# Kernel optimization log

Measured on AMD Instinct MI355X. Metric: run time of the kernel, lower is better.

Reference implementation:

```python
import jax, jax.numpy as jnp
import numpy as np

B, S, D, H = 4, 2048, 1024, 16
HD = D // H  # 64


def setup_inputs() -> dict:
    key = jax.random.key(0)
    ks = jax.random.split(key, 8)
    std = 0.02
    return {
        "input_tensor": jax.random.normal(ks[0], (B, S, D), jnp.float32),
        "attention_mask": jnp.zeros((B, 1, 1, S), jnp.float32),
        "Wq": jax.random.normal(ks[1], (D, D), jnp.float32) * std,
        "bq": jnp.zeros((D,), jnp.float32),
        "Wk": jax.random.normal(ks[2], (D, D), jnp.float32) * std,
        "bk": jnp.zeros((D,), jnp.float32),
        "Wv": jax.random.normal(ks[3], (D, D), jnp.float32) * std,
        "bv": jnp.zeros((D,), jnp.float32),
    }


def reference(input_tensor, attention_mask, Wq, bq, Wk, bk, Wv, bv):
    # QKV projections: [B,S,D]
    q = input_tensor @ Wq + bq
    k = input_tensor @ Wk + bk
    v = input_tensor @ Wv + bv
    # split heads -> [B,H,S,hd]
    split = lambda x: x.reshape(B, S, H, HD).transpose(0, 2, 1, 3)
    q, k, v = split(q), split(k), split(v)
    scale = HD ** (-0.5)
    # [B,H,S,S]
    scores = jnp.einsum("bhqd,bhkd->bhqk", q * scale, k) + attention_mask
    probs = jax.nn.softmax(scores, axis=-1)  # dropout skipped (train=False)
    out = jnp.einsum("bhqk,bhkd->bhqd", probs, v)
    return out.transpose(0, 2, 1, 3).reshape(B, S, D)
```

## Files before the change

### kernel.cpp

```cpp
#include <hip/hip_runtime.h>
#include <hip/hip_bf16.h>

#define BB 4
#define SS 2048
#define DD 1024
#define HH 16
#define HDD 64
#define MM (BB*SS)
#define KVB 64
#define NT (SS/KVB)

typedef __attribute__((ext_vector_type(4))) float f32x4;
typedef __attribute__((ext_vector_type(2))) _Float16 f16x2;
typedef __attribute__((ext_vector_type(4))) _Float16 f16x4;
typedef __attribute__((ext_vector_type(8))) _Float16 f16x8;
typedef __attribute__((ext_vector_type(2))) __fp16 fp16x2_builtin;
typedef __attribute__((ext_vector_type(4))) unsigned int u32x4;

#define LOG2E 1.4426950408889634f
#define QSCALE (0.125f * LOG2E)

__device__ inline float fast_exp2(float x) {
  return __builtin_exp2f(x);
}

__device__ inline f16x2 pk2(float a, float b) {
  union { fp16x2_builtin b2; f16x2 h2; } u;
  u.b2 = __builtin_amdgcn_cvt_pkrtz(a, b);
  return u.h2;
}

__device__ inline f32x4 mfma16(f16x8 a, f16x8 b, f32x4 c) {
  return __builtin_amdgcn_mfma_f32_16x16x32_f16(a, b, c, 0, 0, 0);
}

__device__ inline f16x8 comb(f16x4 lo, f16x4 hi) {
  return __builtin_shufflevector(lo, hi, 0, 1, 2, 3, 4, 5, 6, 7);
}

__device__ inline f16x8 ld_frag(const _Float16* p) {
  f16x4 lo = *reinterpret_cast<const f16x4*>(p);
  f16x4 hi = *reinterpret_cast<const f16x4*>(p + 16);
  return comb(lo, hi);
}

__global__ __launch_bounds__(256) void cvt_x_kernel(
    const float* __restrict__ x, _Float16* __restrict__ xh, int n4) {
  int i = blockIdx.x * 256 + threadIdx.x;
  int stride = gridDim.x * 256;
  for (; i < n4; i += stride) {
    f32x4 v = reinterpret_cast<const f32x4*>(x)[i];
    reinterpret_cast<f16x4*>(xh)[i] = __builtin_convertvector(v, f16x4);
  }
}

__global__ __launch_bounds__(256) void mask_scale_kernel(
    const float* __restrict__ m, float* __restrict__ o, int n) {
  int i = blockIdx.x * 256 + threadIdx.x;
  if (i < n) o[i] = m[i] * LOG2E;
}

__global__ __launch_bounds__(256) void cvt_w_kernel(
    const float* __restrict__ Wq, const float* __restrict__ Wk,
    const float* __restrict__ Wv, _Float16* __restrict__ Wt) {
  __shared__ float tile[32][33];
  const int w = blockIdx.z;
  const float* W = (w == 0) ? Wq : (w == 1) ? Wk : Wv;
  _Float16* outp = Wt + (size_t)w * DD * DD;
  const int n0 = blockIdx.x * 32, k0 = blockIdx.y * 32;
  const int tx = threadIdx.x, ty = threadIdx.y;
#pragma unroll
  for (int i = 0; i < 32; i += 8)
    tile[ty + i][tx] = W[(size_t)(k0 + ty + i) * DD + n0 + tx];
  __syncthreads();
#pragma unroll
  for (int i = 0; i < 32; i += 8)
    outp[(size_t)(n0 + ty + i) * DD + k0 + tx] = (_Float16)tile[tx][ty + i];
}

#define LDT 40
__global__ __launch_bounds__(256) void qkv_gemm_kernel(
    const _Float16* __restrict__ Xh, const _Float16* __restrict__ Wt,
    const float* __restrict__ bq, const float* __restrict__ bk, const float* __restrict__ bv,
    _Float16* __restrict__ Qh, _Float16* __restrict__ Kh,
    _Float16* __restrict__ Vt) {
  __shared__ _Float16 At[128 * LDT];
  __shared__ _Float16 Bt[128 * LDT];
  const int w = blockIdx.y;
  const _Float16* Wp = Wt + (size_t)w * DD * DD;
  const int tid = threadIdx.x;
  const int lane = tid & 63, wave = tid >> 6;
  const int g = lane >> 4, r = lane & 15;
  const int mt = blockIdx.x & 63, nt = blockIdx.x >> 6;
  const int m0 = mt * 128, n0 = nt * 128;
  const int wr = wave >> 1, wc = wave & 1;

  f32x4 acc[4][4];
#pragma unroll
  for (int i = 0; i < 4; ++i)
#pragma unroll
    for (int j = 0; j < 4; ++j) { f32x4 z = {0.f, 0.f, 0.f, 0.f}; acc[i][j] = z; }

  const int r0 = tid >> 2, c0 = (tid & 3) * 8;
  const int r1 = (tid + 256) >> 2, c1 = (tid & 3) * 8;

  u32x4 a0 = *reinterpret_cast<const u32x4*>(&Xh[(size_t)(m0 + r0) * DD + c0]);
  u32x4 a1 = *reinterpret_cast<const u32x4*>(&Xh[(size_t)(m0 + r1) * DD + c1]);
  u32x4 b0 = *reinterpret_cast<const u32x4*>(&Wp[(size_t)(n0 + r0) * DD + c0]);
  u32x4 b1 = *reinterpret_cast<const u32x4*>(&Wp[(size_t)(n0 + r1) * DD + c1]);

  for (int kt = 0; kt < DD; kt += 32) {
    __syncthreads();
    *reinterpret_cast<u32x4*>(&At[r0 * LDT + c0]) = a0;
    *reinterpret_cast<u32x4*>(&At[r1 * LDT + c1]) = a1;
    *reinterpret_cast<u32x4*>(&Bt[r0 * LDT + c0]) = b0;
    *reinterpret_cast<u32x4*>(&Bt[r1 * LDT + c1]) = b1;
    __syncthreads();

    const bool more = (kt + 32) < DD;
    if (more) {
      a0 = *reinterpret_cast<const u32x4*>(&Xh[(size_t)(m0 + r0) * DD + kt + 32 + c0]);
      a1 = *reinterpret_cast<const u32x4*>(&Xh[(size_t)(m0 + r1) * DD + kt + 32 + c1]);
      b0 = *reinterpret_cast<const u32x4*>(&Wp[(size_t)(n0 + r0) * DD + kt + 32 + c0]);
      b1 = *reinterpret_cast<const u32x4*>(&Wp[(size_t)(n0 + r1) * DD + kt + 32 + c1]);
    }

    f16x8 af[4], bf[4];
#pragma unroll
    for (int ms = 0; ms < 4; ++ms)
      af[ms] = ld_frag(&At[(wr * 64 + ms * 16 + r) * LDT + 4 * g]);
#pragma unroll
    for (int ns = 0; ns < 4; ++ns)
      bf[ns] = ld_frag(&Bt[(wc * 64 + ns * 16 + r) * LDT + 4 * g]);
#pragma unroll
    for (int ms = 0; ms < 4; ++ms)
#pragma unroll
      for (int ns = 0; ns < 4; ++ns)
        acc[ms][ns] = mfma16(af[ms], bf[ns], acc[ms][ns]);
  }

  const float* bias = (w == 0) ? bq : (w == 1) ? bk : bv;
#pragma unroll
  for (int ns = 0; ns < 4; ++ns) {
    const int gcol = n0 + wc * 64 + ns * 16 + r;
    const float bv_ = bias[gcol];
    const int h = gcol >> 6, d = gcol & 63;
#pragma unroll
    for (int ms = 0; ms < 4; ++ms) {
#pragma unroll
      for (int reg = 0; reg < 4; ++reg) {
        const int grow = m0 + wr * 64 + ms * 16 + 4 * g + reg;
        const float v = acc[ms][ns][reg] + bv_;
        const int bb = grow >> 11, s = grow & 2047;
        const int bh = bb * HH + h;
        if (w == 0)
          Qh[((size_t)bh * SS + s) * HDD + d] = (_Float16)(v * QSCALE);
        else if (w == 1)
          Kh[((size_t)bh * SS + s) * HDD + d] = (_Float16)v;
        else {
          const int w5 = s & 31;
          const int pos = (w5 & 16) ? ((((w5 >> 2) & 3) << 3) + 4 + (w5 & 3))
                                    : (((w5 >> 2) << 3) + (w5 & 3));
          const int sp = (s & ~31) | pos;
          Vt[((size_t)bh * HDD + d) * SS + sp] = (_Float16)v;
        }
      }
    }
  }
}

__global__ __launch_bounds__(256) void attn_kernel(
    const _Float16* __restrict__ Qh, const _Float16* __restrict__ Kh,
    const _Float16* __restrict__ Vg, const float* __restrict__ maskSc,
    float* __restrict__ out) {
  __shared__ _Float16 Ks[2][KVB * 64];
  __shared__ _Float16 Vs[2][KVB * 64];
  const int bh = blockIdx.y;
  const int b = bh >> 4, h = bh & 15;
  const int tid = threadIdx.x, lane = tid & 63, wave = tid >> 6;
  const int g = lane >> 4, r = lane & 15;
  const int q0 = blockIdx.x * 128 + wave * 32;

  f16x8 qf[2][2];
#pragma unroll
  for (int qs = 0; qs < 2; ++qs) {
    const _Float16* Qp = Qh + ((size_t)bh * SS + q0 + qs * 16 + r) * HDD;
    qf[qs][0] = *reinterpret_cast<const f16x8*>(Qp + 8 * g);
    qf[qs][1] = *reinterpret_cast<const f16x8*>(Qp + 32 + 8 * g);
  }

  float m_run[2] = {-1e30f, -1e30f};
  float l_run[2] = {0.f, 0.f};
  f32x4 acc[2][4];
#pragma unroll
  for (int qs = 0; qs < 2; ++qs)
#pragma unroll
    for (int i = 0; i < 4; ++i) { f32x4 z = {0.f, 0.f, 0.f, 0.f}; acc[qs][i] = z; }

  const _Float16* Kg = Kh + (size_t)bh * SS * HDD;
  const _Float16* Vgb = Vg + (size_t)bh * HDD * SS;
  const float* mbase = maskSc + b * SS;

  const int srow = lane >> 3;
  const int scol = (lane & 7) * 8;
  u32x4 kreg[2], vreg[2];

  auto stage_load = [&](int kk) {
#pragma unroll
    for (int i = 0; i < 2; ++i) {
      const int row = wave * 16 + i * 8 + srow;
      kreg[i] = *reinterpret_cast<const u32x4*>(Kg + (size_t)(kk + row) * HDD + scol);
      vreg[i] = *reinterpret_cast<const u32x4*>(Vgb + (size_t)row * SS + kk + scol);
    }
  };
  auto stage_write = [&](int buf) {
#pragma unroll
    for (int i = 0; i < 2; ++i) {
      const int row = wave * 16 + i * 8 + srow;
      const int sw = (row & 7) << 3;
      *reinterpret_cast<u32x4*>(&Ks[buf][row * 64 + (scol ^ sw)]) = kreg[i];
      *reinterpret_cast<u32x4*>(&Vs[buf][row * 64 + (scol ^ sw)]) = vreg[i];
    }
  };

  int cur = 0;
  stage_load(0);
  stage_write(0);
  __syncthreads();

  for (int t = 0; t < NT; ++t) {
    const int kk = t * KVB;
    const bool more = (t + 1) < NT;
    if (more) stage_load(kk + KVB);

    f32x4 mk[2][2];
#pragma unroll
    for (int sg = 0; sg < 2; ++sg)
#pragma unroll
      for (int h16 = 0; h16 < 2; ++h16)
        mk[sg][h16] = *reinterpret_cast<const f32x4*>(mbase + kk + sg * 32 + h16 * 16 + 4 * g);

#pragma unroll
    for (int sg = 0; sg < 2; ++sg) {
      f32x4 st[2][2];
#pragma unroll
      for (int h16 = 0; h16 < 2; ++h16) {
        const int row = sg * 32 + h16 * 16 + r;
        const int sw = (row & 7) << 3;
        const _Float16* kb = &Ks[cur][row * 64];
        f16x8 a0 = *reinterpret_cast<const f16x8*>(kb + ((8 * g) ^ sw));
        f16x8 a1 = *reinterpret_cast<const f16x8*>(kb + ((32 + 8 * g) ^ sw));
        f32x4 z = {0.f, 0.f, 0.f, 0.f};
        st[0][h16] = mfma16(a1, qf[0][1], mfma16(a0, qf[0][0], z));
        st[1][h16] = mfma16(a1, qf[1][1], mfma16(a0, qf[1][0], z));
      }

      f16x8 pf[2];
#pragma unroll
      for (int qs = 0; qs < 2; ++qs) {
        float p0[4], p1[4];
        float pmax = -1e30f;
#pragma unroll
        for (int j = 0; j < 4; ++j) {
          const float s0 = st[qs][0][j] + mk[sg][0][j];
          const float s1 = st[qs][1][j] + mk[sg][1][j];
          p0[j] = s0; p1[j] = s1;
          pmax = fmaxf(pmax, fmaxf(s0, s1));
        }
        if (!__all(pmax <= m_run[qs] + 8.0f)) {
          float tm = fmaxf(pmax, __shfl_xor(pmax, 16));
          tm = fmaxf(tm, __shfl_xor(tm, 32));
          const float m_new = fmaxf(m_run[qs], tm);
          const float corr = fast_exp2(m_run[qs] - m_new);
          l_run[qs] *= corr;
#pragma unroll
          for (int i = 0; i < 4; ++i) acc[qs][i] = acc[qs][i] * corr;
          m_run[qs] = m_new;
        }
        const float mr = m_run[qs];
        float rs = 0.f;
#pragma unroll
        for (int j = 0; j < 4; ++j) {
          p0[j] = fast_exp2(p0[j] - mr);
          p1[j] = fast_exp2(p1[j] - mr);
          rs += p0[j] + p1[j];
        }
        l_run[qs] += rs;
        union { f16x2 h2[4]; f16x8 v; } u;
        u.h2[0] = pk2(p0[0], p0[1]);
        u.h2[1] = pk2(p0[2], p0[3]);
        u.h2[2] = pk2(p1[0], p1[1]);
        u.h2[3] = pk2(p1[2], p1[3]);
        pf[qs] = u.v;
      }

#pragma unroll
      for (int dsb = 0; dsb < 4; ++dsb) {
        const int row = dsb * 16 + r;
        const int sw = (row & 7) << 3;
        f16x8 vf = *reinterpret_cast<const f16x8*>(
            &Vs[cur][row * 64 + ((sg * 32 + 8 * g) ^ sw)]);
        acc[0][dsb] = mfma16(vf, pf[0], acc[0][dsb]);
        acc[1][dsb] = mfma16(vf, pf[1], acc[1][dsb]);
      }
    }

    if (more) stage_write(cur ^ 1);
    __syncthreads();
    cur ^= 1;
  }

#pragma unroll
  for (int qs = 0; qs < 2; ++qs) {
    float l = l_run[qs];
    l += __shfl_xor(l, 16);
    l += __shfl_xor(l, 32);
    const float inv = 1.0f / l;
    float* op = out + ((size_t)b * SS + q0 + qs * 16 + r) * DD + h * HDD;
#pragma unroll
    for (int dsb = 0; dsb < 4; ++dsb) {
      f32x4 o = { acc[qs][dsb][0] * inv, acc[qs][dsb][1] * inv,
                  acc[qs][dsb][2] * inv, acc[qs][dsb][3] * inv };
      *reinterpret_cast<f32x4*>(op + dsb * 16 + 4 * g) = o;
    }
  }
}

extern "C" void kernel_launch(void* const* d_in, const int* in_sizes, int n_in,
                              void* d_out, int out_size, void* d_ws, size_t ws_size,
                              hipStream_t stream) {
  const float* x    = (const float*)d_in[0];
  const float* mask = (const float*)d_in[1];
  const float* Wq   = (const float*)d_in[2];
  const float* bq   = (const float*)d_in[3];
  const float* Wk   = (const float*)d_in[4];
  const float* bk   = (const float*)d_in[5];
  const float* Wv   = (const float*)d_in[6];
  const float* bv   = (const float*)d_in[7];
  float* out = (float*)d_out;

  _Float16* Xh = (_Float16*)d_ws;
  _Float16* Wt = Xh + (size_t)MM * DD;
  _Float16* Qh = Wt + (size_t)3 * DD * DD;
  _Float16* Kh = Qh + (size_t)MM * DD;
  _Float16* Vt = Kh + (size_t)MM * DD;
  float* maskSc = (float*)(Vt + (size_t)MM * DD);

  cvt_x_kernel<<<dim3(2048), dim3(256), 0, stream>>>(x, Xh, MM * DD / 4);
  mask_scale_kernel<<<dim3((BB * SS + 255) / 256), dim3(256), 0, stream>>>(mask, maskSc, BB * SS);
  cvt_w_kernel<<<dim3(32, 32, 3), dim3(32, 8), 0, stream>>>(Wq, Wk, Wv, Wt);
  qkv_gemm_kernel<<<dim3(512, 3), dim3(256), 0, stream>>>(Xh, Wt, bq, bk, bv, Qh, Kh, Vt);
  attn_kernel<<<dim3(SS / 128, BB * HH), dim3(256), 0, stream>>>(Qh, Kh, Vt, maskSc, out);
}
```

Baseline: 340.9 us.

## Use direct global-to-LDS loads with double buffering in GEMM and attention

The QKV GEMM switches from register-staged loads into a padded shared tile to double-buffered global_load_lds copies into XOR-swizzled tiles. It also replaces split 4-element fragment loads with single 8-element loads. The attention kernel likewise uses direct global-to-LDS prefetch of K/V tiles and moves to 512 threads, with each wave handling 16 query rows instead of 32. The aim is to cut register staging and VGPR pressure, overlap loads with MFMA work, and raise occupancy. The cost is that each K/V tile in LDS is reused by fewer query rows per wave, and correctness depends on the swizzle matching the layout that global_load_lds writes.

```diff
diff --git a/kernel.cpp b/kernel.cpp
--- a/kernel.cpp
+++ b/kernel.cpp
@@ -15,14 +15,11 @@
 typedef __attribute__((ext_vector_type(4))) _Float16 f16x4;
 typedef __attribute__((ext_vector_type(8))) _Float16 f16x8;
 typedef __attribute__((ext_vector_type(2))) __fp16 fp16x2_builtin;
-typedef __attribute__((ext_vector_type(4))) unsigned int u32x4;
 
 #define LOG2E 1.4426950408889634f
 #define QSCALE (0.125f * LOG2E)
 
-__device__ inline float fast_exp2(float x) {
-  return __builtin_exp2f(x);
-}
+__device__ inline float fast_exp2(float x) { return __builtin_exp2f(x); }
 
 __device__ inline f16x2 pk2(float a, float b) {
   union { fp16x2_builtin b2; f16x2 h2; } u;
@@ -30,18 +27,14 @@
   return u.h2;
 }
 
+__device__ inline void glds16(const void* g, void* l) {
+  __builtin_amdgcn_global_load_lds(
+      (__attribute__((address_space(1))) void*)(g),
+      (__attribute__((address_space(3))) void*)(l), 16, 0, 0);
+}
+
 __device__ inline f32x4 mfma16(f16x8 a, f16x8 b, f32x4 c) {
   return __builtin_amdgcn_mfma_f32_16x16x32_f16(a, b, c, 0, 0, 0);
-}
-
-__device__ inline f16x8 comb(f16x4 lo, f16x4 hi) {
-  return __builtin_shufflevector(lo, hi, 0, 1, 2, 3, 4, 5, 6, 7);
-}
-
-__device__ inline f16x8 ld_frag(const _Float16* p) {
-  f16x4 lo = *reinterpret_cast<const f16x4*>(p);
-  f16x4 hi = *reinterpret_cast<const f16x4*>(p + 16);
-  return comb(lo, hi);
 }
 
 __global__ __launch_bounds__(256) void cvt_x_kernel(
@@ -78,14 +71,13 @@
     outp[(size_t)(n0 + ty + i) * DD + k0 + tx] = (_Float16)tile[tx][ty + i];
 }
 
-#define LDT 40
 __global__ __launch_bounds__(256) void qkv_gemm_kernel(
     const _Float16* __restrict__ Xh, const _Float16* __restrict__ Wt,
     const float* __restrict__ bq, const float* __restrict__ bk, const float* __restrict__ bv,
     _Float16* __restrict__ Qh, _Float16* __restrict__ Kh,
     _Float16* __restrict__ Vt) {
-  __shared__ _Float16 At[128 * LDT];
-  __shared__ _Float16 Bt[128 * LDT];
+  __shared__ _Float16 At[2][128 * 32];
+  __shared__ _Float16 Bt[2][128 * 32];
   const int w = blockIdx.y;
   const _Float16* Wp = Wt + (size_t)w * DD * DD;
   const int tid = threadIdx.x;
@@ -101,42 +93,40 @@
 #pragma unroll
     for (int j = 0; j < 4; ++j) { f32x4 z = {0.f, 0.f, 0.f, 0.f}; acc[i][j] = z; }
 
-  const int r0 = tid >> 2, c0 = (tid & 3) * 8;
-  const int r1 = (tid + 256) >> 2, c1 = (tid & 3) * 8;
-
-  u32x4 a0 = *reinterpret_cast<const u32x4*>(&Xh[(size_t)(m0 + r0) * DD + c0]);
-  u32x4 a1 = *reinterpret_cast<const u32x4*>(&Xh[(size_t)(m0 + r1) * DD + c1]);
-  u32x4 b0 = *reinterpret_cast<const u32x4*>(&Wp[(size_t)(n0 + r0) * DD + c0]);
-  u32x4 b1 = *reinterpret_cast<const u32x4*>(&Wp[(size_t)(n0 + r1) * DD + c1]);
-
+  const int srow = lane >> 2;
+  const int scol = 8 * ((lane & 3) ^ (srow & 3));
+  const int cA = (8 * g) ^ (8 * (r & 3));
+
+  auto stage = [&](int kt, int buf) {
+#pragma unroll
+    for (int i = 0; i < 2; ++i) {
+      const int c = wave * 2 + i;
+      glds16(Xh + (size_t)(m0 + 16 * c + srow) * DD + kt + scol, &At[buf][c * 512]);
+      glds16(Wp + (size_t)(n0 + 16 * c + srow) * DD + kt + scol, &Bt[buf][c * 512]);
+    }
+  };
+
+  stage(0, 0);
+  __syncthreads();
+  int buf = 0;
   for (int kt = 0; kt < DD; kt += 32) {
-    __syncthreads();
-    *reinterpret_cast<u32x4*>(&At[r0 * LDT + c0]) = a0;
-    *reinterpret_cast<u32x4*>(&At[r1 * LDT + c1]) = a1;
-    *reinterpret_cast<u32x4*>(&Bt[r0 * LDT + c0]) = b0;
-    *reinterpret_cast<u32x4*>(&Bt[r1 * LDT + c1]) = b1;
-    __syncthreads();
-
-    const bool more = (kt + 32) < DD;
-    if (more) {
-      a0 = *reinterpret_cast<const u32x4*>(&Xh[(size_t)(m0 + r0) * DD + kt + 32 + c0]);
-      a1 = *reinterpret_cast<const u32x4*>(&Xh[(size_t)(m0 + r1) * DD + kt + 32 + c1]);
-      b0 = *reinterpret_cast<const u32x4*>(&Wp[(size_t)(n0 + r0) * DD + kt + 32 + c0]);
-      b1 = *reinterpret_cast<const u32x4*>(&Wp[(size_t)(n0 + r1) * DD + kt + 32 + c1]);
-    }
+    if (kt + 32 < DD) stage(kt + 32, buf ^ 1);
 
     f16x8 af[4], bf[4];
 #pragma unroll
     for (int ms = 0; ms < 4; ++ms)
-      af[ms] = ld_frag(&At[(wr * 64 + ms * 16 + r) * LDT + 4 * g]);
+      af[ms] = *reinterpret_cast<const f16x8*>(&At[buf][(wr * 64 + ms * 16 + r) * 32 + cA]);
 #pragma unroll
     for (int ns = 0; ns < 4; ++ns)
-      bf[ns] = ld_frag(&Bt[(wc * 64 + ns * 16 + r) * LDT + 4 * g]);
+      bf[ns] = *reinterpret_cast<const f16x8*>(&Bt[buf][(wc * 64 + ns * 16 + r) * 32 + cA]);
 #pragma unroll
     for (int ms = 0; ms < 4; ++ms)
 #pragma unroll
       for (int ns = 0; ns < 4; ++ns)
         acc[ms][ns] = mfma16(af[ms], bf[ns], acc[ms][ns]);
+
+    __syncthreads();
+    buf ^= 1;
   }
 
   const float* bias = (w == 0) ? bq : (w == 1) ? bk : bv;
@@ -169,7 +159,7 @@
   }
 }
 
-__global__ __launch_bounds__(256) void attn_kernel(
+__global__ __launch_bounds__(512) void attn_kernel(
     const _Float16* __restrict__ Qh, const _Float16* __restrict__ Kh,
     const _Float16* __restrict__ Vg, const float* __restrict__ maskSc,
     float* __restrict__ out) {
@@ -177,61 +167,45 @@
   __shared__ _Float16 Vs[2][KVB * 64];
   const int bh = blockIdx.y;
   const int b = bh >> 4, h = bh & 15;
-  const int tid = threadIdx.x, lane = tid & 63, wave = tid >> 6;
+  const int tid = threadIdx.x, lane = tid & 63, w = tid >> 6;
   const int g = lane >> 4, r = lane & 15;
-  const int q0 = blockIdx.x * 128 + wave * 32;
-
-  f16x8 qf[2][2];
-#pragma unroll
-  for (int qs = 0; qs < 2; ++qs) {
-    const _Float16* Qp = Qh + ((size_t)bh * SS + q0 + qs * 16 + r) * HDD;
-    qf[qs][0] = *reinterpret_cast<const f16x8*>(Qp + 8 * g);
-    qf[qs][1] = *reinterpret_cast<const f16x8*>(Qp + 32 + 8 * g);
-  }
-
-  float m_run[2] = {-1e30f, -1e30f};
-  float l_run[2] = {0.f, 0.f};
-  f32x4 acc[2][4];
-#pragma unroll
-  for (int qs = 0; qs < 2; ++qs)
-#pragma unroll
-    for (int i = 0; i < 4; ++i) { f32x4 z = {0.f, 0.f, 0.f, 0.f}; acc[qs][i] = z; }
+  const int q0 = blockIdx.x * 128 + w * 16;
 
   const _Float16* Kg = Kh + (size_t)bh * SS * HDD;
   const _Float16* Vgb = Vg + (size_t)bh * HDD * SS;
   const float* mbase = maskSc + b * SS;
 
-  const int srow = lane >> 3;
-  const int scol = (lane & 7) * 8;
-  u32x4 kreg[2], vreg[2];
-
-  auto stage_load = [&](int kk) {
-#pragma unroll
-    for (int i = 0; i < 2; ++i) {
-      const int row = wave * 16 + i * 8 + srow;
-      kreg[i] = *reinterpret_cast<const u32x4*>(Kg + (size_t)(kk + row) * HDD + scol);
-      vreg[i] = *reinterpret_cast<const u32x4*>(Vgb + (size_t)row * SS + kk + scol);
-    }
+  const _Float16* Qp = Qh + ((size_t)bh * SS + q0 + r) * HDD;
+  const f16x8 qf0 = *reinterpret_cast<const f16x8*>(Qp + 8 * g);
+  const f16x8 qf1 = *reinterpret_cast<const f16x8*>(Qp + 32 + 8 * g);
+
+  float m_run = -1e30f, l_run = 0.f;
+  f32x4 acc[4];
+#pragma unroll
+  for (int i = 0; i < 4; ++i) { f32x4 z = {0.f, 0.f, 0.f, 0.f}; acc[i] = z; }
+
+  const int sr = lane >> 3;
+  const int sc = 8 * ((lane & 7) ^ sr);
+  const _Float16* kSrc = Kg + (size_t)(w * 8 + sr) * HDD + sc;
+  const _Float16* vSrc = Vgb + (size_t)(w * 8 + sr) * SS + sc;
+  const int wdst = w * 512;
+
+  const int c0 = (8 * g) ^ (8 * (r & 7));
+
+  auto prefetch = [&](int t, int buf) {
+    const int kk = t * KVB;
+    glds16(kSrc + (size_t)kk * HDD, &Ks[buf][wdst]);
+    glds16(vSrc + kk, &Vs[buf][wdst]);
   };
-  auto stage_write = [&](int buf) {
-#pragma unroll
-    for (int i = 0; i < 2; ++i) {
-      const int row = wave * 16 + i * 8 + srow;
-      const int sw = (row & 7) << 3;
-      *reinterpret_cast<u32x4*>(&Ks[buf][row * 64 + (scol ^ sw)]) = kreg[i];
-      *reinterpret_cast<u32x4*>(&Vs[buf][row * 64 + (scol ^ sw)]) = vreg[i];
-    }
-  };
-
-  int cur = 0;
-  stage_load(0);
-  stage_write(0);
+
+  prefetch(0, 0);
   __syncthreads();
 
   for (int t = 0; t < NT; ++t) {
+    if (t + 1 < NT) prefetch(t + 1, (t + 1) & 1);
+    const _Float16* kb = &Ks[t & 1][0];
+    const _Float16* vb = &Vs[t & 1][0];
     const int kk = t * KVB;
-    const bool more = (t + 1) < NT;
-    if (more) stage_load(kk + KVB);
 
     f32x4 mk[2][2];
 #pragma unroll
@@ -242,87 +216,72 @@
 
 #pragma unroll
     for (int sg = 0; sg < 2; ++sg) {
-      f32x4 st[2][2];
+      f32x4 st[2];
 #pragma unroll
       for (int h16 = 0; h16 < 2; ++h16) {
         const int row = sg * 32 + h16 * 16 + r;
-        const int sw = (row & 7) << 3;
-        const _Float16* kb = &Ks[cur][row * 64];
-        f16x8 a0 = *reinterpret_cast<const f16x8*>(kb + ((8 * g) ^ sw));
-        f16x8 a1 = *reinterpret_cast<const f16x8*>(kb + ((32 + 8 * g) ^ sw));
+        f16x8 a0 = *reinterpret_cast<const f16x8*>(kb + row * 64 + c0);
+        f16x8 a1 = *reinterpret_cast<const f16x8*>(kb + row * 64 + (c0 ^ 32));
         f32x4 z = {0.f, 0.f, 0.f, 0.f};
-        st[0][h16] = mfma16(a1, qf[0][1], mfma16(a0, qf[0][0], z));
-        st[1][h16] = mfma16(a1, qf[1][1], mfma16(a0, qf[1][0], z));
-      }
-
-      f16x8 pf[2];
-#pragma unroll
-      for (int qs = 0; qs < 2; ++qs) {
-        float p0[4], p1[4];
-        float pmax = -1e30f;
-#pragma unroll
-        for (int j = 0; j < 4; ++j) {
-          const float s0 = st[qs][0][j] + mk[sg][0][j];
-          const float s1 = st[qs][1][j] + mk[sg][1][j];
-          p0[j] = s0; p1[j] = s1;
-          pmax = fmaxf(pmax, fmaxf(s0, s1));
-        }
-        if (!__all(pmax <= m_run[qs] + 8.0f)) {
-          float tm = fmaxf(pmax, __shfl_xor(pmax, 16));
-          tm = fmaxf(tm, __shfl_xor(tm, 32));
-          const float m_new = fmaxf(m_run[qs], tm);
-          const float corr = fast_exp2(m_run[qs] - m_new);
-          l_run[qs] *= corr;
-#pragma unroll
-          for (int i = 0; i < 4; ++i) acc[qs][i] = acc[qs][i] * corr;
-          m_run[qs] = m_new;
-        }
-        const float mr = m_run[qs];
-        float rs = 0.f;
-#pragma unroll
-        for (int j = 0; j < 4; ++j) {
-          p0[j] = fast_exp2(p0[j] - mr);
-          p1[j] = fast_exp2(p1[j] - mr);
-          rs += p0[j] + p1[j];
-        }
-        l_run[qs] += rs;
-        union { f16x2 h2[4]; f16x8 v; } u;
-        u.h2[0] = pk2(p0[0], p0[1]);
-        u.h2[1] = pk2(p0[2], p0[3]);
-        u.h2[2] = pk2(p1[0], p1[1]);
-        u.h2[3] = pk2(p1[2], p1[3]);
-        pf[qs] = u.v;
-      }
+        st[h16] = mfma16(a1, qf1, mfma16(a0, qf0, z));
+      }
+
+      float p0[4], p1[4];
+      float pmax = -1e30f;
+#pragma unroll
+      for (int j = 0; j < 4; ++j) {
+        const float s0 = st[0][j] + mk[sg][0][j];
+        const float s1 = st[1][j] + mk[sg][1][j];
+        p0[j] = s0; p1[j] = s1;
+        pmax = fmaxf(pmax, fmaxf(s0, s1));
+      }
+      if (!__all(pmax <= m_run + 8.0f)) {
+        float tm = fmaxf(pmax, __shfl_xor(pmax, 16));
+        tm = fmaxf(tm, __shfl_xor(tm, 32));
+        const float m_new = fmaxf(m_run, tm);
+        const float corr = fast_exp2(m_run - m_new);
+        l_run *= corr;
+#pragma unroll
+        for (int i = 0; i < 4; ++i) acc[i] = acc[i] * corr;
+        m_run = m_new;
+      }
+      const float mr = m_run;
+      float rs = 0.f;
+#pragma unroll
+      for (int j = 0; j < 4; ++j) {
+        p0[j] = fast_exp2(p0[j] - mr);
+        p1[j] = fast_exp2(p1[j] - mr);
+        rs += p0[j] + p1[j];
+      }
+      l_run += rs;
+      union { f16x2 h2[4]; f16x8 v; } u;
+      u.h2[0] = pk2(p0[0], p0[1]);
+      u.h2[1] = pk2(p0[2], p0[3]);
+      u.h2[2] = pk2(p1[0], p1[1]);
+      u.h2[3] = pk2(p1[2], p1[3]);
+      const f16x8 pf = u.v;
 
 #pragma unroll
       for (int dsb = 0; dsb < 4; ++dsb) {
-        const int row = dsb * 16 + r;
-        const int sw = (row & 7) << 3;
-        f16x8 vf = *reinterpret_cast<const f16x8*>(
-            &Vs[cur][row * 64 + ((sg * 32 + 8 * g) ^ sw)]);
-        acc[0][dsb] = mfma16(vf, pf[0], acc[0][dsb]);
-        acc[1][dsb] = mfma16(vf, pf[1], acc[1][dsb]);
+        const int vrow = dsb * 16 + r;
+        f16x8 vf = *reinterpret_cast<const f16x8*>(vb + vrow * 64 + (c0 ^ (sg * 32)));
+        acc[dsb] = mfma16(vf, pf, acc[dsb]);
       }
     }
 
-    if (more) stage_write(cur ^ 1);
     __syncthreads();
-    cur ^= 1;
-  }
-
-#pragma unroll
-  for (int qs = 0; qs < 2; ++qs) {
-    float l = l_run[qs];
-    l += __shfl_xor(l, 16);
-    l += __shfl_xor(l, 32);
-    const float inv = 1.0f / l;
-    float* op = out + ((size_t)b * SS + q0 + qs * 16 + r) * DD + h * HDD;
-#pragma unroll
-    for (int dsb = 0; dsb < 4; ++dsb) {
-      f32x4 o = { acc[qs][dsb][0] * inv, acc[qs][dsb][1] * inv,
-                  acc[qs][dsb][2] * inv, acc[qs][dsb][3] * inv };
-      *reinterpret_cast<f32x4*>(op + dsb * 16 + 4 * g) = o;
-    }
+  }
+
+  float l = l_run;
+  l += __shfl_xor(l, 16);
+  l += __shfl_xor(l, 32);
+  const float inv = 1.0f / l;
+  float* op = out + ((size_t)b * SS + q0 + r) * DD + h * HDD;
+#pragma unroll
+  for (int dsb = 0; dsb < 4; ++dsb) {
+    f32x4 o = { acc[dsb][0] * inv, acc[dsb][1] * inv,
+                acc[dsb][2] * inv, acc[dsb][3] * inv };
+    *reinterpret_cast<f32x4*>(op + dsb * 16 + 4 * g) = o;
   }
 }
 
@@ -350,5 +309,5 @@
   mask_scale_kernel<<<dim3((BB * SS + 255) / 256), dim3(256), 0, stream>>>(mask, maskSc, BB * SS);
   cvt_w_kernel<<<dim3(32, 32, 3), dim3(32, 8), 0, stream>>>(Wq, Wk, Wv, Wt);
   qkv_gemm_kernel<<<dim3(512, 3), dim3(256), 0, stream>>>(Xh, Wt, bq, bk, bv, Qh, Kh, Vt);
-  attn_kernel<<<dim3(SS / 128, BB * HH), dim3(256), 0, stream>>>(Qh, Kh, Vt, maskSc, out);
-}
+  attn_kernel<<<dim3(SS / 128, BB * HH), dim3(512), 0, stream>>>(Qh, Kh, Vt, maskSc, out);
+}
```

New measurement: 324.0 us. 1.05x faster.
